# Kernel tuning notes

Measured on AMD Instinct MI355X. Metric: run time of the kernel, lower is better.

## Reference

```python
import math
import jax, jax.numpy as jnp
import numpy as np

S, M, B, D, H = 256, 256, 8, 512, 8
HD = D // H
K = S + M  # key_len


def setup_inputs() -> dict:
    key = jax.random.key(0)
    ks = jax.random.split(key, 10)
    x = jax.random.normal(ks[0], (S, B, D), jnp.float32)
    memory = jax.random.normal(ks[1], (M, B, D), jnp.float32)
    rel_pos = jax.random.normal(ks[2], (K, D), jnp.float32)
    # causal mask: True means masked (key position after query position)
    q_pos = jnp.arange(S)[:, None] + M  # (S,1)
    k_pos = jnp.arange(K)[None, :]     # (1,K)
    attn_mask = jnp.broadcast_to(k_pos > q_pos, (B, S, K))
    scale = 1.0 / math.sqrt(D)
    Wq = jax.random.normal(ks[3], (D, D), jnp.float32) * scale
    Wk = jax.random.normal(ks[4], (D, D), jnp.float32) * scale
    Wv = jax.random.normal(ks[5], (D, D), jnp.float32) * scale
    Wr = jax.random.normal(ks[6], (D, D), jnp.float32) * scale
    Wo = jax.random.normal(ks[7], (D, D), jnp.float32) * scale
    u_bias = jax.random.normal(ks[8], (H, HD), jnp.float32) * 0.02
    v_bias = jax.random.normal(ks[9], (H, HD), jnp.float32) * 0.02
    return {"x": x, "memory": memory, "rel_pos": rel_pos, "attn_mask": attn_mask,
            "Wq": Wq, "Wk": Wk, "Wv": Wv, "Wr": Wr, "Wo": Wo,
            "u_bias": u_bias, "v_bias": v_bias}


def reference(x, memory, rel_pos, attn_mask, Wq, Wk, Wv, Wr, Wo, u_bias, v_bias):
    mem = jax.lax.stop_gradient(memory)
    kv = jnp.concatenate([mem, x], axis=0)  # (K, B, D)
    # projections (torch Linear: y = x @ W.T)
    q = (x @ Wq.T).reshape(S, B, H, HD).transpose(1, 2, 0, 3)   # (B,H,S,HD)
    k = (kv @ Wk.T).reshape(K, B, H, HD).transpose(1, 2, 0, 3)  # (B,H,K,HD)
    v = (kv @ Wv.T).reshape(K, B, H, HD).transpose(1, 2, 0, 3)  # (B,H,K,HD)
    r = (rel_pos[:K] @ Wr.T).reshape(K, H, HD)                  # (K,H,HD)
    # relative index gather
    q_pos = jnp.arange(S)[:, None] + M
    k_pos = jnp.arange(K)[None, :]
    rel_idx = jnp.clip(q_pos - k_pos, 0, K - 1)  # (S,K)
    r_qk = r[rel_idx]                            # (S,K,H,HD)
    qk = jnp.einsum('bhqd,bhkd->bhqk', q, k)
    qr = jnp.einsum('bhqd,qkhd->bhqk', q, r_qk)
    uk = jnp.einsum('hd,bhkd->bhk', u_bias, k)[:, :, None, :]
    vr = jnp.einsum('hd,qkhd->hqk', v_bias, r_qk)[None]
    scores = (qk + qr + uk + vr) / math.sqrt(HD)  # (B,H,S,K)
    scores = jnp.where(attn_mask[:, None, :, :], -jnp.inf, scores)
    weights = jax.nn.softmax(scores, axis=-1)
    y = jnp.einsum('bhqk,bhkd->bhqd', weights, v)
    y = y.transpose(2, 0, 1, 3).reshape(S, B, D)
    return y @ Wo.T
```

## Files before the change

kernel.cpp:

```cpp
#include <hip/hip_runtime.h>
#include <math.h>

constexpr int S_  = 256;
constexpr int Mm  = 256;
constexpr int Bb  = 8;
constexpr int Dd  = 512;
constexpr int Hh  = 8;
constexpr int HDd = 64;
constexpr int Kk  = 512;

typedef unsigned short u16;
typedef short bf16x8 __attribute__((ext_vector_type(8)));
typedef float f32x4  __attribute__((ext_vector_type(4)));

constexpr int LROW = 72;
constexpr int QSTR = 520;

__device__ __forceinline__ u16 f2b(float f) {
  union { float f; unsigned int u; } v; v.f = f;
  unsigned int u = v.u + 0x7fffu + ((v.u >> 16) & 1u);
  return (u16)(u >> 16);
}
__device__ __forceinline__ float b2f(u16 b) {
  union { unsigned int u; float f; } v; v.u = ((unsigned int)b) << 16;
  return v.f;
}

__device__ __forceinline__ void stage_bf16(u16* dst, const u16* __restrict__ src,
                                           int ld, int tid) {
  const int r = tid >> 3, c = (tid & 7) * 8;
  *(int4*)(dst + r * LROW + c)        = *(const int4*)(src + (size_t)r * ld + c);
  *(int4*)(dst + (r + 32) * LROW + c) = *(const int4*)(src + (size_t)(r + 32) * ld + c);
}
__device__ __forceinline__ void stage_f32(u16* dst, const float* __restrict__ src,
                                          int ld, int tid, int nrow32) {
  const int r = tid >> 3, c = (tid & 7) * 8;
  for (int hh = 0; hh < nrow32; ++hh) {
    const float4 a = *(const float4*)(src + (size_t)(r + 32 * hh) * ld + c);
    const float4 b = *(const float4*)(src + (size_t)(r + 32 * hh) * ld + c + 4);
    union { u16 u[8]; int4 v; } p;
    p.u[0] = f2b(a.x); p.u[1] = f2b(a.y); p.u[2] = f2b(a.z); p.u[3] = f2b(a.w);
    p.u[4] = f2b(b.x); p.u[5] = f2b(b.y); p.u[6] = f2b(b.z); p.u[7] = f2b(b.w);
    *(int4*)(dst + (r + 32 * hh) * LROW + c) = p.v;
  }
}

__device__ __forceinline__ void mfma_step(const u16* As, const u16* Bs,
                                          f32x4 (&acc)[4], int wave, int lane) {
  const int r16 = lane & 15, q8 = (lane >> 4) * 8;
#pragma unroll
  for (int ks = 0; ks < 64; ks += 32) {
    const bf16x8 a = *(const bf16x8*)(As + (wave * 16 + r16) * LROW + ks + q8);
#pragma unroll
    for (int nb = 0; nb < 4; ++nb) {
      const bf16x8 b = *(const bf16x8*)(Bs + (nb * 16 + r16) * LROW + ks + q8);
      acc[nb] = __builtin_amdgcn_mfma_f32_16x16x32_bf16(a, b, acc[nb], 0, 0, 0);
    }
  }
}

__global__ __launch_bounds__(256) void k_proj(const float* __restrict__ x,
                                              const float* __restrict__ mem,
                                              const float* __restrict__ rel,
                                              const float* __restrict__ Wq,
                                              const float* __restrict__ Wk,
                                              const float* __restrict__ Wv,
                                              const float* __restrict__ Wr,
                                              const float* __restrict__ ub,
                                              const float* __restrict__ vb,
                                              u16* __restrict__ qu,
                                              u16* __restrict__ qv,
                                              u16* __restrict__ kb,
                                              u16* __restrict__ vT,
                                              u16* __restrict__ rT) {
  __shared__ u16 As[128 * LROW], Bs[64 * LROW];
  const int tid = threadIdx.x, wave = tid >> 6, lane = tid & 63;
  const int r16 = lane & 15, q8 = (lane >> 4) * 8, rq = (lane >> 4) * 4;
  const int bid = blockIdx.x;
  int kind, mt, nt;
  const float *A, *B;
  if (bid < 128)      { kind = 0; int t = bid;       mt = t >> 3; nt = t & 7; B = Wq; }
  else if (bid < 384) { kind = 1; int t = bid - 128; mt = t >> 3; nt = t & 7; B = Wk; }
  else if (bid < 640) { kind = 2; int t = bid - 384; mt = t >> 3; nt = t & 7; B = Wv; }
  else                { kind = 3; int t = bid - 640; mt = t >> 3; nt = t & 7; B = Wr; }
  const int m0 = mt * 128, n0 = nt * 64;
  if (kind == 0)      A = x + (size_t)m0 * Dd;
  else if (kind == 3) A = rel + (size_t)m0 * Dd;
  else                A = (m0 < Mm * Bb) ? mem + (size_t)m0 * Dd
                                         : x + (size_t)(m0 - Mm * Bb) * Dd;
  B += (size_t)n0 * Dd;

  f32x4 acc[2][4];
#pragma unroll
  for (int mi = 0; mi < 2; ++mi)
#pragma unroll
    for (int nb = 0; nb < 4; ++nb) acc[mi][nb] = (f32x4){0.f, 0.f, 0.f, 0.f};

  for (int k0 = 0; k0 < Dd; k0 += 64) {
    stage_f32(As, A + k0, Dd, tid, 4);
    stage_f32(Bs, B + k0, Dd, tid, 2);
    __syncthreads();
#pragma unroll
    for (int ks = 0; ks < 64; ks += 32) {
      bf16x8 a[2];
#pragma unroll
      for (int mi = 0; mi < 2; ++mi)
        a[mi] = *(const bf16x8*)(As + (wave * 32 + mi * 16 + r16) * LROW + ks + q8);
#pragma unroll
      for (int nb = 0; nb < 4; ++nb) {
        const bf16x8 bb = *(const bf16x8*)(Bs + (nb * 16 + r16) * LROW + ks + q8);
#pragma unroll
        for (int mi = 0; mi < 2; ++mi)
          acc[mi][nb] = __builtin_amdgcn_mfma_f32_16x16x32_bf16(a[mi], bb, acc[mi][nb], 0, 0, 0);
      }
    }
    __syncthreads();
  }

  const int h = n0 >> 6;
  if (kind == 0) {
#pragma unroll
    for (int nb = 0; nb < 4; ++nb) {
      const int hd = nb * 16 + r16, n = n0 + hd;
      const float u = ub[n], v = vb[n];
#pragma unroll
      for (int mi = 0; mi < 2; ++mi)
#pragma unroll
        for (int r = 0; r < 4; ++r) {
          const int m = m0 + wave * 32 + mi * 16 + rq + r;
          const int s = m >> 3, b = m & 7;
          const size_t d = ((size_t)(b * Hh + h) * S_ + s) * HDd + hd;
          qu[d] = f2b(acc[mi][nb][r] + u);
          qv[d] = f2b(acc[mi][nb][r] + v);
        }
    }
  } else if (kind == 1) {
#pragma unroll
    for (int nb = 0; nb < 4; ++nb) {
      const int hd = nb * 16 + r16;
#pragma unroll
      for (int mi = 0; mi < 2; ++mi)
#pragma unroll
        for (int r = 0; r < 4; ++r) {
          const int m = m0 + wave * 32 + mi * 16 + rq + r;
          const int pos = m >> 3, b = m & 7;
          kb[((size_t)(b * Hh + h) * Kk + pos) * HDd + hd] = f2b(acc[mi][nb][r]);
        }
    }
  } else if (kind == 2) {
#pragma unroll
    for (int nb = 0; nb < 4; ++nb) {
      const int hd = nb * 16 + r16;
#pragma unroll
      for (int mi = 0; mi < 2; ++mi)
#pragma unroll
        for (int r = 0; r < 4; ++r) {
          const int m = m0 + wave * 32 + mi * 16 + rq + r;
          const int pos = m >> 3, b = m & 7;
          vT[((size_t)(b * Hh + h) * HDd + hd) * Kk + pos] = f2b(acc[mi][nb][r]);
        }
    }
  } else {
#pragma unroll
    for (int nb = 0; nb < 4; ++nb) {
      const int hd = nb * 16 + r16;
#pragma unroll
      for (int mi = 0; mi < 2; ++mi)
#pragma unroll
        for (int r = 0; r < 4; ++r) {
          const int j = m0 + wave * 32 + mi * 16 + rq + r;
          rT[((size_t)h * Kk + j) * HDd + hd] = f2b(acc[mi][nb][r]);
        }
    }
  }
}

__global__ __launch_bounds__(256) void k_attn(const u16* __restrict__ qu,
                                              const u16* __restrict__ qv,
                                              const u16* __restrict__ kb,
                                              const u16* __restrict__ vT,
                                              const u16* __restrict__ rT,
                                              u16* __restrict__ y) {
  extern __shared__ u16 lds[];
  u16* QRP = lds;
  u16* Bs0 = lds + 64 * QSTR;
  u16* Bs1 = Bs0 + 64 * LROW;
  const int tid = threadIdx.x, wave = tid >> 6, lane = tid & 63;
  const int q0 = blockIdx.x * 64, bh = blockIdx.y, h = bh & 7, b = bh >> 3;
  const int r16 = lane & 15, q8 = (lane >> 4) * 8, rq = (lane >> 4) * 4;
  const int sr = tid >> 3, scg = (tid & 7) * 8;

  const u16* qvp = qv + ((size_t)bh * S_ + q0 + wave * 16 + r16) * HDd;
  const bf16x8 av0 = *(const bf16x8*)(qvp + q8);
  const bf16x8 av1 = *(const bf16x8*)(qvp + 32 + q8);
  const u16* qup = qu + ((size_t)bh * S_ + q0 + wave * 16 + r16) * HDd;
  const bf16x8 au0 = *(const bf16x8*)(qup + q8);
  const bf16x8 au1 = *(const bf16x8*)(qup + 32 + q8);

  const u16* rbase = rT + (size_t)h * Kk * HDd;
  const u16* kbase = kb + (size_t)bh * Kk * HDd;
  const u16* vbase = vT + (size_t)bh * HDd * Kk;

  f32x4 sc[8][4];
  f32x4 o[4];
#pragma unroll
  for (int nb = 0; nb < 4; ++nb) o[nb] = (f32x4){0.f, 0.f, 0.f, 0.f};
  float mx[4]  = {-INFINITY, -INFINITY, -INFINITY, -INFINITY};

  *(int4*)(Bs0 + sr * LROW + scg) =
      *(const int4*)(rbase + (size_t)sr * HDd + scg);
  *(int4*)(Bs0 + (sr + 32) * LROW + scg) =
      *(const int4*)(rbase + (size_t)(sr + 32) * HDd + scg);
  __syncthreads();

#pragma unroll
  for (int j = 0; j < 24; ++j) {
    int4 L0, L1;
    if (j < 23) {
      const int jn = j + 1;
      const u16* s;
      int ld;
      if (jn < 8)       { s = rbase + (size_t)(jn * 64) * HDd;       ld = HDd; }
      else if (jn < 16) { s = kbase + (size_t)((jn - 8) * 64) * HDd; ld = HDd; }
      else              { s = vbase + (jn - 16) * 64;                ld = Kk;  }
      L0 = *(const int4*)(s + (size_t)sr * ld + scg);
      L1 = *(const int4*)(s + (size_t)(sr + 32) * ld + scg);
    }
    const u16* buf = (j & 1) ? Bs1 : Bs0;

    if (j < 8) {
      f32x4 c4[4];
#pragma unroll
      for (int nb = 0; nb < 4; ++nb) c4[nb] = (f32x4){0.f, 0.f, 0.f, 0.f};
#pragma unroll
      for (int ks = 0; ks < 64; ks += 32) {
        const bf16x8 a = ks ? av1 : av0;
#pragma unroll
        for (int nb = 0; nb < 4; ++nb) {
          const bf16x8 bb = *(const bf16x8*)(buf + (nb * 16 + r16) * LROW + ks + q8);
          c4[nb] = __builtin_amdgcn_mfma_f32_16x16x32_bf16(a, bb, c4[nb], 0, 0, 0);
        }
      }
#pragma unroll
      for (int nb = 0; nb < 4; ++nb)
#pragma unroll
        for (int r = 0; r < 4; ++r)
          QRP[(wave * 16 + rq + r) * QSTR + j * 64 + nb * 16 + r16] = f2b(c4[nb][r]);
    } else if (j < 16) {
      const int t = j - 8;
#pragma unroll
      for (int nb = 0; nb < 4; ++nb) sc[t][nb] = (f32x4){0.f, 0.f, 0.f, 0.f};
#pragma unroll
      for (int ks = 0; ks < 64; ks += 32) {
        const bf16x8 a = ks ? au1 : au0;
#pragma unroll
        for (int nb = 0; nb < 4; ++nb) {
          const bf16x8 bb = *(const bf16x8*)(buf + (nb * 16 + r16) * LROW + ks + q8);
          sc[t][nb] = __builtin_amdgcn_mfma_f32_16x16x32_bf16(a, bb, sc[t][nb], 0, 0, 0);
        }
      }
      if (j == 15) {
#pragma unroll
        for (int kt = 0; kt < 8; ++kt)
#pragma unroll
          for (int nb = 0; nb < 4; ++nb) {
            const int kk = kt * 64 + nb * 16 + r16;
#pragma unroll
            for (int r = 0; r < 4; ++r) {
              const int ql = wave * 16 + rq + r;
              const int q  = q0 + ql;
              float v;
              if (kk <= q + Mm) {
                const float qr = b2f(QRP[ql * QSTR + (q + Mm - kk)]);
                v = (sc[kt][nb][r] + qr) * 0.125f;
              } else {
                v = -INFINITY;
              }
              sc[kt][nb][r] = v;
              mx[r] = fmaxf(mx[r], v);
            }
          }
#pragma unroll
        for (int r = 0; r < 4; ++r)
#pragma unroll
          for (int off = 1; off < 16; off <<= 1)
            mx[r] = fmaxf(mx[r], __shfl_xor(mx[r], off));
        float sum[4] = {0.f, 0.f, 0.f, 0.f};
#pragma unroll
        for (int kt = 0; kt < 8; ++kt)
#pragma unroll
          for (int nb = 0; nb < 4; ++nb)
#pragma unroll
            for (int r = 0; r < 4; ++r) {
              const float p = __expf(sc[kt][nb][r] - mx[r]);
              sc[kt][nb][r] = p;
              sum[r] += p;
            }
#pragma unroll
        for (int r = 0; r < 4; ++r)
#pragma unroll
          for (int off = 1; off < 16; off <<= 1) sum[r] += __shfl_xor(sum[r], off);
        float inv[4];
#pragma unroll
        for (int r = 0; r < 4; ++r) inv[r] = 1.0f / sum[r];
#pragma unroll
        for (int kt = 0; kt < 8; ++kt)
#pragma unroll
          for (int nb = 0; nb < 4; ++nb)
#pragma unroll
            for (int r = 0; r < 4; ++r)
              QRP[(wave * 16 + rq + r) * QSTR + kt * 64 + nb * 16 + r16] =
                  f2b(sc[kt][nb][r] * inv[r]);
      }
    } else {
      const int t = j - 16;
#pragma unroll
      for (int ks = 0; ks < 64; ks += 32) {
        const bf16x8 a = *(const bf16x8*)(QRP + (wave * 16 + r16) * QSTR + t * 64 + ks + q8);
#pragma unroll
        for (int nb = 0; nb < 4; ++nb) {
          const bf16x8 bb = *(const bf16x8*)(buf + (nb * 16 + r16) * LROW + ks + q8);
          o[nb] = __builtin_amdgcn_mfma_f32_16x16x32_bf16(a, bb, o[nb], 0, 0, 0);
        }
      }
    }

    if (j < 23) {
      u16* d = ((j + 1) & 1) ? Bs1 : Bs0;
      *(int4*)(d + sr * LROW + scg)        = L0;
      *(int4*)(d + (sr + 32) * LROW + scg) = L1;
    }
    __syncthreads();
  }

#pragma unroll
  for (int nb = 0; nb < 4; ++nb) {
    const int hd = nb * 16 + r16;
#pragma unroll
    for (int r = 0; r < 4; ++r) {
      const int q = q0 + wave * 16 + rq + r;
      y[((size_t)q * Bb + b) * Dd + h * HDd + hd] = f2b(o[nb][r]);
    }
  }
}

__global__ __launch_bounds__(256) void k_out(const u16* __restrict__ y,
                                             const float* __restrict__ Wo,
                                             float* __restrict__ out) {
  __shared__ u16 As[2][64 * LROW], Bs[2][64 * LROW];
  const int tid = threadIdx.x, wave = tid >> 6, lane = tid & 63;
  const int n0 = blockIdx.x * 64, m0 = blockIdx.y * 64;
  const int sr = tid >> 3, scg = (tid & 7) * 8;
  const u16* Ay = y + (size_t)m0 * Dd;
  const float* Bw = Wo + (size_t)n0 * Dd;
  f32x4 acc[4];
#pragma unroll
  for (int i = 0; i < 4; ++i) acc[i] = (f32x4){0.f, 0.f, 0.f, 0.f};

  stage_bf16(As[0], Ay, Dd, tid);
  stage_f32(Bs[0], Bw, Dd, tid, 2);
  __syncthreads();

#pragma unroll
  for (int t = 0; t < 8; ++t) {
    int4 La0, La1;
    float4 f0, f1, f2, f3;
    if (t < 7) {
      const u16* s = Ay + (t + 1) * 64;
      La0 = *(const int4*)(s + (size_t)sr * Dd + scg);
      La1 = *(const int4*)(s + (size_t)(sr + 32) * Dd + scg);
      const float* w = Bw + (t + 1) * 64;
      f0 = *(const float4*)(w + (size_t)sr * Dd + scg);
      f1 = *(const float4*)(w + (size_t)sr * Dd + scg + 4);
      f2 = *(const float4*)(w + (size_t)(sr + 32) * Dd + scg);
      f3 = *(const float4*)(w + (size_t)(sr + 32) * Dd + scg + 4);
    }
    mfma_step(As[t & 1], Bs[t & 1], acc, wave, lane);
    if (t < 7) {
      u16* da = As[(t + 1) & 1];
      *(int4*)(da + sr * LROW + scg)        = La0;
      *(int4*)(da + (sr + 32) * LROW + scg) = La1;
      u16* db = Bs[(t + 1) & 1];
      union { u16 u[8]; int4 v; } p;
      p.u[0] = f2b(f0.x); p.u[1] = f2b(f0.y); p.u[2] = f2b(f0.z); p.u[3] = f2b(f0.w);
      p.u[4] = f2b(f1.x); p.u[5] = f2b(f1.y); p.u[6] = f2b(f1.z); p.u[7] = f2b(f1.w);
      *(int4*)(db + sr * LROW + scg) = p.v;
      p.u[0] = f2b(f2.x); p.u[1] = f2b(f2.y); p.u[2] = f2b(f2.z); p.u[3] = f2b(f2.w);
      p.u[4] = f2b(f3.x); p.u[5] = f2b(f3.y); p.u[6] = f2b(f3.z); p.u[7] = f2b(f3.w);
      *(int4*)(db + (sr + 32) * LROW + scg) = p.v;
    }
    __syncthreads();
  }

  const int r16 = lane & 15, rq = (lane >> 4) * 4;
#pragma unroll
  for (int nb = 0; nb < 4; ++nb) {
    const int n = n0 + nb * 16 + r16;
#pragma unroll
    for (int r = 0; r < 4; ++r) {
      const int m = m0 + wave * 16 + rq + r;
      out[(size_t)m * Dd + n] = acc[nb][r];
    }
  }
}

extern "C" void kernel_launch(void* const* d_in, const int* in_sizes, int n_in,
                              void* d_out, int out_size, void* d_ws, size_t ws_size,
                              hipStream_t stream) {
  const float* x    = (const float*)d_in[0];
  const float* mem  = (const float*)d_in[1];
  const float* rel  = (const float*)d_in[2];
  const float* Wq = (const float*)d_in[4];
  const float* Wk = (const float*)d_in[5];
  const float* Wv = (const float*)d_in[6];
  const float* Wr = (const float*)d_in[7];
  const float* Wo = (const float*)d_in[8];
  const float* ub = (const float*)d_in[9];
  const float* vb = (const float*)d_in[10];
  float* out = (float*)d_out;

  u16* qu = (u16*)d_ws;
  u16* qv = qu + 1048576;
  u16* kb = qv + 1048576;
  u16* vT = kb + 2097152;
  u16* rT = vT + 2097152;
  u16* yb = rT + 262144;

  constexpr int ATTN_LDS = (64 * QSTR + 2 * 64 * LROW) * (int)sizeof(u16);
  (void)hipFuncSetAttribute((const void*)k_attn,
                            hipFuncAttributeMaxDynamicSharedMemorySize, ATTN_LDS);

  k_proj<<<dim3(672),   dim3(256), 0,        stream>>>(x, mem, rel, Wq, Wk, Wv, Wr,
                                                       ub, vb, qu, qv, kb, vT, rT);
  k_attn<<<dim3(4, 64), dim3(256), ATTN_LDS, stream>>>(qu, qv, kb, vT, rT, yb);
  k_out <<<dim3(8, 32), dim3(256), 0,        stream>>>(yb, Wo, out);
}
```

Measured before the change: 141.9 us.

## Fuse K and V projections per block and register-prefetch next k-tile

The projection kernel now computes K and V together in one block, so the shared activation tile (memory/x) is loaded and converted to bf16 once instead of twice, and the grid shrinks from 672 to 416 blocks. The main loop also prefetches the next k-tile into registers while MFMAs run on the current LDS tile, hiding global load latency. In exchange the kernel uses more registers (two accumulator sets plus prefetch buffers) and more LDS, which may lower occupancy, and K/V blocks now carry roughly double the work of the Q and R blocks.

After: 137.5 us. 1.03x faster.

```diff
diff --git a/kernel.cpp b/kernel.cpp
--- a/kernel.cpp
+++ b/kernel.cpp
@@ -25,6 +25,12 @@
   union { unsigned int u; float f; } v; v.u = ((unsigned int)b) << 16;
   return v.f;
 }
+__device__ __forceinline__ int4 pack8(float4 a, float4 b) {
+  union { u16 u[8]; int4 v; } p;
+  p.u[0] = f2b(a.x); p.u[1] = f2b(a.y); p.u[2] = f2b(a.z); p.u[3] = f2b(a.w);
+  p.u[4] = f2b(b.x); p.u[5] = f2b(b.y); p.u[6] = f2b(b.z); p.u[7] = f2b(b.w);
+  return p.v;
+}
 
 __device__ __forceinline__ void stage_bf16(u16* dst, const u16* __restrict__ src,
                                            int ld, int tid) {
@@ -38,10 +44,7 @@
   for (int hh = 0; hh < nrow32; ++hh) {
     const float4 a = *(const float4*)(src + (size_t)(r + 32 * hh) * ld + c);
     const float4 b = *(const float4*)(src + (size_t)(r + 32 * hh) * ld + c + 4);
-    union { u16 u[8]; int4 v; } p;
-    p.u[0] = f2b(a.x); p.u[1] = f2b(a.y); p.u[2] = f2b(a.z); p.u[3] = f2b(a.w);
-    p.u[4] = f2b(b.x); p.u[5] = f2b(b.y); p.u[6] = f2b(b.z); p.u[7] = f2b(b.w);
-    *(int4*)(dst + (r + 32 * hh) * LROW + c) = p.v;
+    *(int4*)(dst + (r + 32 * hh) * LROW + c) = pack8(a, b);
   }
 }
 
@@ -73,33 +76,85 @@
                                               u16* __restrict__ kb,
                                               u16* __restrict__ vT,
                                               u16* __restrict__ rT) {
-  __shared__ u16 As[128 * LROW], Bs[64 * LROW];
+  __shared__ u16 As[128 * LROW], Bs[64 * LROW], Bs2[64 * LROW];
   const int tid = threadIdx.x, wave = tid >> 6, lane = tid & 63;
   const int r16 = lane & 15, q8 = (lane >> 4) * 8, rq = (lane >> 4) * 4;
+  const int sr = tid >> 3, scg = (tid & 7) * 8;
   const int bid = blockIdx.x;
   int kind, mt, nt;
-  const float *A, *B;
-  if (bid < 128)      { kind = 0; int t = bid;       mt = t >> 3; nt = t & 7; B = Wq; }
-  else if (bid < 384) { kind = 1; int t = bid - 128; mt = t >> 3; nt = t & 7; B = Wk; }
-  else if (bid < 640) { kind = 2; int t = bid - 384; mt = t >> 3; nt = t & 7; B = Wv; }
-  else                { kind = 3; int t = bid - 640; mt = t >> 3; nt = t & 7; B = Wr; }
+  if (bid < 128)      { kind = 0; const int t = bid;       mt = t >> 3; nt = t & 7; }
+  else if (bid < 384) { kind = 1; const int t = bid - 128; mt = t >> 3; nt = t & 7; }
+  else                { kind = 2; const int t = bid - 384; mt = t >> 3; nt = t & 7; }
   const int m0 = mt * 128, n0 = nt * 64;
-  if (kind == 0)      A = x + (size_t)m0 * Dd;
-  else if (kind == 3) A = rel + (size_t)m0 * Dd;
-  else                A = (m0 < Mm * Bb) ? mem + (size_t)m0 * Dd
-                                         : x + (size_t)(m0 - Mm * Bb) * Dd;
-  B += (size_t)n0 * Dd;
-
-  f32x4 acc[2][4];
+  const float *A, *B, *B2 = nullptr;
+  if (kind == 0)      { A = x + (size_t)m0 * Dd; B = Wq + (size_t)n0 * Dd; }
+  else if (kind == 1) { A = (m0 < Mm * Bb) ? mem + (size_t)m0 * Dd
+                                           : x + (size_t)(m0 - Mm * Bb) * Dd;
+                        B = Wk + (size_t)n0 * Dd; B2 = Wv + (size_t)n0 * Dd; }
+  else                { A = rel + (size_t)m0 * Dd; B = Wr + (size_t)n0 * Dd; }
+
+  f32x4 accK[2][4], accV[2][4];
 #pragma unroll
   for (int mi = 0; mi < 2; ++mi)
 #pragma unroll
-    for (int nb = 0; nb < 4; ++nb) acc[mi][nb] = (f32x4){0.f, 0.f, 0.f, 0.f};
+    for (int nb = 0; nb < 4; ++nb) {
+      accK[mi][nb] = (f32x4){0.f, 0.f, 0.f, 0.f};
+      accV[mi][nb] = (f32x4){0.f, 0.f, 0.f, 0.f};
+    }
+
+  float4 fa[8], fb[4], fv[4];
+#pragma unroll
+  for (int hh = 0; hh < 4; ++hh) {
+    fa[2 * hh]     = *(const float4*)(A + (size_t)(sr + 32 * hh) * Dd + scg);
+    fa[2 * hh + 1] = *(const float4*)(A + (size_t)(sr + 32 * hh) * Dd + scg + 4);
+  }
+#pragma unroll
+  for (int hh = 0; hh < 2; ++hh) {
+    fb[2 * hh]     = *(const float4*)(B + (size_t)(sr + 32 * hh) * Dd + scg);
+    fb[2 * hh + 1] = *(const float4*)(B + (size_t)(sr + 32 * hh) * Dd + scg + 4);
+  }
+  if (kind == 1) {
+#pragma unroll
+    for (int hh = 0; hh < 2; ++hh) {
+      fv[2 * hh]     = *(const float4*)(B2 + (size_t)(sr + 32 * hh) * Dd + scg);
+      fv[2 * hh + 1] = *(const float4*)(B2 + (size_t)(sr + 32 * hh) * Dd + scg + 4);
+    }
+  }
+#pragma unroll
+  for (int hh = 0; hh < 4; ++hh)
+    *(int4*)(As + (sr + 32 * hh) * LROW + scg) = pack8(fa[2 * hh], fa[2 * hh + 1]);
+#pragma unroll
+  for (int hh = 0; hh < 2; ++hh)
+    *(int4*)(Bs + (sr + 32 * hh) * LROW + scg) = pack8(fb[2 * hh], fb[2 * hh + 1]);
+  if (kind == 1) {
+#pragma unroll
+    for (int hh = 0; hh < 2; ++hh)
+      *(int4*)(Bs2 + (sr + 32 * hh) * LROW + scg) = pack8(fv[2 * hh], fv[2 * hh + 1]);
+  }
+  __syncthreads();
 
   for (int k0 = 0; k0 < Dd; k0 += 64) {
-    stage_f32(As, A + k0, Dd, tid, 4);
-    stage_f32(Bs, B + k0, Dd, tid, 2);
-    __syncthreads();
+    const bool more = k0 < Dd - 64;
+    if (more) {
+      const int kn = k0 + 64;
+#pragma unroll
+      for (int hh = 0; hh < 4; ++hh) {
+        fa[2 * hh]     = *(const float4*)(A + (size_t)(sr + 32 * hh) * Dd + kn + scg);
+        fa[2 * hh + 1] = *(const float4*)(A + (size_t)(sr + 32 * hh) * Dd + kn + scg + 4);
+      }
+#pragma unroll
+      for (int hh = 0; hh < 2; ++hh) {
+        fb[2 * hh]     = *(const float4*)(B + (size_t)(sr + 32 * hh) * Dd + kn + scg);
+        fb[2 * hh + 1] = *(const float4*)(B + (size_t)(sr + 32 * hh) * Dd + kn + scg + 4);
+      }
+      if (kind == 1) {
+#pragma unroll
+        for (int hh = 0; hh < 2; ++hh) {
+          fv[2 * hh]     = *(const float4*)(B2 + (size_t)(sr + 32 * hh) * Dd + kn + scg);
+          fv[2 * hh + 1] = *(const float4*)(B2 + (size_t)(sr + 32 * hh) * Dd + kn + scg + 4);
+        }
+      }
+    }
 #pragma unroll
     for (int ks = 0; ks < 64; ks += 32) {
       bf16x8 a[2];
@@ -108,13 +163,33 @@
         a[mi] = *(const bf16x8*)(As + (wave * 32 + mi * 16 + r16) * LROW + ks + q8);
 #pragma unroll
       for (int nb = 0; nb < 4; ++nb) {
-        const bf16x8 bb = *(const bf16x8*)(Bs + (nb * 16 + r16) * LROW + ks + q8);
+        const bf16x8 bk = *(const bf16x8*)(Bs + (nb * 16 + r16) * LROW + ks + q8);
 #pragma unroll
         for (int mi = 0; mi < 2; ++mi)
-          acc[mi][nb] = __builtin_amdgcn_mfma_f32_16x16x32_bf16(a[mi], bb, acc[mi][nb], 0, 0, 0);
+          accK[mi][nb] = __builtin_amdgcn_mfma_f32_16x16x32_bf16(a[mi], bk, accK[mi][nb], 0, 0, 0);
+        if (kind == 1) {
+          const bf16x8 bv = *(const bf16x8*)(Bs2 + (nb * 16 + r16) * LROW + ks + q8);
+#pragma unroll
+          for (int mi = 0; mi < 2; ++mi)
+            accV[mi][nb] = __builtin_amdgcn_mfma_f32_16x16x32_bf16(a[mi], bv, accV[mi][nb], 0, 0, 0);
+        }
       }
     }
     __syncthreads();
+    if (more) {
+#pragma unroll
+      for (int hh = 0; hh < 4; ++hh)
+        *(int4*)(As + (sr + 32 * hh) * LROW + scg) = pack8(fa[2 * hh], fa[2 * hh + 1]);
+#pragma unroll
+      for (int hh = 0; hh < 2; ++hh)
+        *(int4*)(Bs + (sr + 32 * hh) * LROW + scg) = pack8(fb[2 * hh], fb[2 * hh + 1]);
+      if (kind == 1) {
+#pragma unroll
+        for (int hh = 0; hh < 2; ++hh)
+          *(int4*)(Bs2 + (sr + 32 * hh) * LROW + scg) = pack8(fv[2 * hh], fv[2 * hh + 1]);
+      }
+      __syncthreads();
+    }
   }
 
   const int h = n0 >> 6;
@@ -130,8 +205,8 @@
           const int m = m0 + wave * 32 + mi * 16 + rq + r;
           const int s = m >> 3, b = m & 7;
           const size_t d = ((size_t)(b * Hh + h) * S_ + s) * HDd + hd;
-          qu[d] = f2b(acc[mi][nb][r] + u);
-          qv[d] = f2b(acc[mi][nb][r] + v);
+          qu[d] = f2b(accK[mi][nb][r] + u);
+          qv[d] = f2b(accK[mi][nb][r] + v);
         }
     }
   } else if (kind == 1) {
@@ -144,10 +219,11 @@
         for (int r = 0; r < 4; ++r) {
           const int m = m0 + wave * 32 + mi * 16 + rq + r;
           const int pos = m >> 3, b = m & 7;
-          kb[((size_t)(b * Hh + h) * Kk + pos) * HDd + hd] = f2b(acc[mi][nb][r]);
-        }
-    }
-  } else if (kind == 2) {
+          kb[((size_t)(b * Hh + h) * Kk + pos) * HDd + hd] = f2b(accK[mi][nb][r]);
+          vT[((size_t)(b * Hh + h) * HDd + hd) * Kk + pos] = f2b(accV[mi][nb][r]);
+        }
+    }
+  } else {
 #pragma unroll
     for (int nb = 0; nb < 4; ++nb) {
       const int hd = nb * 16 + r16;
@@ -155,21 +231,8 @@
       for (int mi = 0; mi < 2; ++mi)
 #pragma unroll
         for (int r = 0; r < 4; ++r) {
-          const int m = m0 + wave * 32 + mi * 16 + rq + r;
-          const int pos = m >> 3, b = m & 7;
-          vT[((size_t)(b * Hh + h) * HDd + hd) * Kk + pos] = f2b(acc[mi][nb][r]);
-        }
-    }
-  } else {
-#pragma unroll
-    for (int nb = 0; nb < 4; ++nb) {
-      const int hd = nb * 16 + r16;
-#pragma unroll
-      for (int mi = 0; mi < 2; ++mi)
-#pragma unroll
-        for (int r = 0; r < 4; ++r) {
           const int j = m0 + wave * 32 + mi * 16 + rq + r;
-          rT[((size_t)h * Kk + j) * HDd + hd] = f2b(acc[mi][nb][r]);
+          rT[((size_t)h * Kk + j) * HDd + hd] = f2b(accK[mi][nb][r]);
         }
     }
   }
@@ -381,13 +444,8 @@
       *(int4*)(da + sr * LROW + scg)        = La0;
       *(int4*)(da + (sr + 32) * LROW + scg) = La1;
       u16* db = Bs[(t + 1) & 1];
-      union { u16 u[8]; int4 v; } p;
-      p.u[0] = f2b(f0.x); p.u[1] = f2b(f0.y); p.u[2] = f2b(f0.z); p.u[3] = f2b(f0.w);
-      p.u[4] = f2b(f1.x); p.u[5] = f2b(f1.y); p.u[6] = f2b(f1.z); p.u[7] = f2b(f1.w);
-      *(int4*)(db + sr * LROW + scg) = p.v;
-      p.u[0] = f2b(f2.x); p.u[1] = f2b(f2.y); p.u[2] = f2b(f2.z); p.u[3] = f2b(f2.w);
-      p.u[4] = f2b(f3.x); p.u[5] = f2b(f3.y); p.u[6] = f2b(f3.z); p.u[7] = f2b(f3.w);
-      *(int4*)(db + (sr + 32) * LROW + scg) = p.v;
+      *(int4*)(db + sr * LROW + scg)        = pack8(f0, f1);
+      *(int4*)(db + (sr + 32) * LROW + scg) = pack8(f2, f3);
     }
     __syncthreads();
   }
@@ -430,7 +488,7 @@
   (void)hipFuncSetAttribute((const void*)k_attn,
                             hipFuncAttributeMaxDynamicSharedMemorySize, ATTN_LDS);
 
-  k_proj<<<dim3(672),   dim3(256), 0,        stream>>>(x, mem, rel, Wq, Wk, Wv, Wr,
+  k_proj<<<dim3(416),   dim3(256), 0,        stream>>>(x, mem, rel, Wq, Wk, Wv, Wr,
                                                        ub, vb, qu, qv, kb, vT, rT);
   k_attn<<<dim3(4, 64), dim3(256), ATTN_LDS, stream>>>(qu, qv, kb, vT, rT, yb);
   k_out <<<dim3(8, 32), dim3(256), 0,        stream>>>(yb, Wo, out);
```
